# Performance work log

Measured on AMD Instinct MI355X. Metric: run time of the kernel, lower is better.

## Reference

```python
import jax, jax.numpy as jnp
import numpy as np

M = 8        # number of input features
NMF = 4      # membership functions per feature
R = NMF ** M # 65536 rules
N = 1024     # batch size


def setup_inputs() -> dict:
    key = jax.random.key(0)
    k1, k2, k3, k4, k5 = jax.random.split(key, 5)
    x = jax.random.normal(k1, (N, M), dtype=jnp.float32)
    # Antecedent parameters: torch.rand -> uniform [0,1)
    center = jax.random.uniform(k2, (M, NMF), dtype=jnp.float32)
    sigma = jax.random.uniform(k3, (M, NMF), dtype=jnp.float32)
    # Consequent linear layer, init_Consequent uses uniform [0,1)
    W = jax.random.uniform(k4, (R, M), dtype=jnp.float32)
    b = jax.random.uniform(k5, (R,), dtype=jnp.float32)
    return {"x": x, "center": center, "sigma": sigma, "W": W, "b": b}


def reference(x, center, sigma, W, b):
    # droprule=False (deterministic reference; the torch drop_rule is random Bernoulli masking)
    n = x.shape[0]
    # Gaussian membership, faithful to torch: exp(-(x - c)^2 / 2 * sigma^2)
    # mg: [N, M, NMF]
    mg = jnp.exp(-((x[:, :, None] - center[None, :, :]) ** 2) * 0.5 * (sigma[None, :, :] ** 2))
    # Combinatorial rule product via mixed-radix broadcasting:
    # fg[n, r] = prod_m mg[n, m, digit_m(r)], feature 0 most significant.
    fg = mg[:, 0, :]  # [N, NMF]
    for m in range(1, M):
        fg = (fg[:, :, None] * mg[:, m, None, :]).reshape(n, -1)
    # fg: [N, R]
    fg_bar = fg / jnp.sum(fg, axis=1, keepdims=True)
    rule_out = x @ W.T + b  # [N, R]
    return jnp.sum(fg_bar * rule_out, axis=1)  # [N]
```

## Files before the change

kernel.cpp:

```cpp
#include <hip/hip_runtime.h>
#include <hip/hip_bf16.h>

typedef __attribute__((ext_vector_type(8))) short short8;
typedef __attribute__((ext_vector_type(4))) float f32x4;

#define KB 16

__device__ __forceinline__ ushort f2bf(float f) {
    __hip_bfloat16 h = __float2bfloat16(f);
    return *reinterpret_cast<ushort*>(&h);
}
__device__ __forceinline__ unsigned pk2(float a, float b) {
    return (unsigned)f2bf(a) | ((unsigned)f2bf(b) << 16);
}

__global__ __launch_bounds__(256) void fz_main(
    const float* __restrict__ x, const float* __restrict__ center,
    const float* __restrict__ sigma, const float* __restrict__ W,
    const float* __restrict__ b, float* __restrict__ out, int N)
{
    __shared__ float  xs[16][9];
    __shared__ float  mgs[16][33];
    __shared__ float  pr[16][20] __attribute__((aligned(16)));
    __shared__ ushort plf[8][64][8] __attribute__((aligned(16)));
    __shared__ float  phs[KB][20] __attribute__((aligned(16)));
    __shared__ float  red[4][16][9];
    __shared__ ushort wstg[2][32][16][8] __attribute__((aligned(16)));

    const int t = threadIdx.x;
    const int tile = blockIdx.x >> 4;
    const int kb = blockIdx.x & (KB - 1);

    if (t < 128) {
        int s = t >> 3, m = t & 7;
        xs[s][m] = x[(size_t)(tile * 16 + s) * 8 + m];
    }
    __syncthreads();
    #pragma unroll
    for (int v = 0; v < 2; ++v) {
        int id = t + v * 256;
        int s = id >> 5, i = id & 31, m = i >> 2;
        float d = xs[s][m] - center[i];
        float sg = sigma[i];
        mgs[s][i] = __expf(-d * d * 0.5f * sg * sg);
    }
    __syncthreads();
    {
        int s = t >> 4, a = t & 15;
        pr[s][a] = mgs[s][24 + (a >> 2)] * mgs[s][28 + (a & 3)];
    }
    {
        int hil = t >> 4, s = t & 15;
        int hi = kb * KB + hil;
        phs[hil][s] = mgs[s][hi >> 6] * mgs[s][4 + ((hi >> 4) & 3)]
                    * mgs[s][8 + ((hi >> 2) & 3)] * mgs[s][12 + (hi & 3)];
    }
    __syncthreads();
    {
        const int ls = t >> 5;
        #pragma unroll
        for (int oct = 0; oct < 2; ++oct) {
            const int lane_e = (2 * t + oct) & 63;
            const int s = lane_e & 15;
            const int hi3 = lane_e >> 4;
            const int L0 = ls * 32 + hi3 * 8;
            const float pqv = mgs[s][16 + (L0 >> 6)] * mgs[s][20 + ((L0 >> 4) & 3)];
            const int b7 = L0 & 8;
            const float4 r0 = *reinterpret_cast<const float4*>(&pr[s][b7]);
            const float4 r1 = *reinterpret_cast<const float4*>(&pr[s][b7 + 4]);
            unsigned Pk[4] = { pk2(pqv * r0.x, pqv * r0.y), pk2(pqv * r0.z, pqv * r0.w),
                               pk2(pqv * r1.x, pqv * r1.y), pk2(pqv * r1.z, pqv * r1.w) };
            *reinterpret_cast<short8*>(&plf[ls][lane_e][0]) =
                *reinterpret_cast<short8*>(&Pk[0]);
        }
    }

    const int wv = t >> 6, lane = t & 63;
    const int c = lane & 15, kb4 = lane >> 4;
    const int srow = t >> 1, shalf = (t & 1) * 4;

    auto stage_load = [&](int hil, float4& va, float4& vb, float& bv) {
        const float* wp = W + (size_t)(kb * KB + hil) * 2048;
        va = *reinterpret_cast<const float4*>(wp + t * 4);
        vb = *reinterpret_cast<const float4*>(wp + 1024 + t * 4);
        bv = b[(kb * KB + hil) * 256 + t];
    };
    auto stage_write = [&](int bf, const float4& va, const float4& vb, float bv) {
        ushort* p0 = &wstg[bf][srow >> 3][shalf][srow & 7];
        p0[0] = f2bf(va.x); p0[8] = f2bf(va.y); p0[16] = f2bf(va.z); p0[24] = f2bf(va.w);
        ushort* p1 = &wstg[bf][16 + (srow >> 3)][shalf][srow & 7];
        p1[0] = f2bf(vb.x); p1[8] = f2bf(vb.y); p1[16] = f2bf(vb.z); p1[24] = f2bf(vb.w);
        wstg[bf][t >> 3][8][t & 7] = f2bf(bv);
    };

    __syncthreads();
    short8 A0 = *reinterpret_cast<const short8*>(&plf[2 * wv][lane][0]);
    short8 A1 = *reinterpret_cast<const short8*>(&plf[2 * wv + 1][lane][0]);

    float4 va, vb2; float bv;
    stage_load(0, va, vb2, bv);
    stage_write(0, va, vb2, bv);
    __syncthreads();

    f32x4 master = {0.f, 0.f, 0.f, 0.f};
    #pragma unroll 2
    for (int hil = 0; hil < KB; ++hil) {
        const int bf = hil & 1;
        if (hil + 1 < KB) stage_load(hil + 1, va, vb2, bv);
        f32x4 d = {0.f, 0.f, 0.f, 0.f};
        short8 B0 = *reinterpret_cast<const short8*>(&wstg[bf][(2 * wv) * 4 + kb4][c][0]);
        short8 B1 = *reinterpret_cast<const short8*>(&wstg[bf][(2 * wv + 1) * 4 + kb4][c][0]);
        d = __builtin_amdgcn_mfma_f32_16x16x32_bf16(A0, B0, d, 0, 0, 0);
        d = __builtin_amdgcn_mfma_f32_16x16x32_bf16(A1, B1, d, 0, 0, 0);
        const float4 phv = *reinterpret_cast<const float4*>(&phs[hil][kb4 * 4]);
        master[0] += phv.x * d[0]; master[1] += phv.y * d[1];
        master[2] += phv.z * d[2]; master[3] += phv.w * d[3];
        if (hil + 1 < KB) stage_write(bf ^ 1, va, vb2, bv);
        __syncthreads();
    }

    if (c < 9) {
        #pragma unroll
        for (int r = 0; r < 4; ++r)
            red[wv][kb4 * 4 + r][c] = master[r];
    }
    __syncthreads();
    if (t < 144) {
        int s = t / 9, cc = t % 9;
        red[0][s][cc] += red[1][s][cc] + red[2][s][cc] + red[3][s][cc];
    }
    __syncthreads();
    if (t < 16) {
        const int s = t;
        float denom = 1.f;
        #pragma unroll
        for (int m = 0; m < 8; ++m)
            denom *= (mgs[s][4 * m] + mgs[s][4 * m + 1] +
                      mgs[s][4 * m + 2] + mgs[s][4 * m + 3]);
        float num = red[0][s][8];
        #pragma unroll
        for (int m = 0; m < 8; ++m) num += xs[s][m] * red[0][s][m];
        atomicAdd(&out[tile * 16 + s], num / denom);
    }
}

extern "C" void kernel_launch(void* const* d_in, const int* in_sizes, int n_in,
                              void* d_out, int out_size, void* d_ws, size_t ws_size,
                              hipStream_t stream)
{
    const float* x      = (const float*)d_in[0];
    const float* center = (const float*)d_in[1];
    const float* sigma  = (const float*)d_in[2];
    const float* W      = (const float*)d_in[3];
    const float* b      = (const float*)d_in[4];
    float* out = (float*)d_out;
    const int N = in_sizes[0] / 8;

    hipMemsetAsync(out, 0, (size_t)out_size * sizeof(float), stream);
    fz_main<<<(N / 16) * KB, 256, 0, stream>>>(x, center, sigma, W, b, out, N);
}
```

Before: 74.27 us.

## Give each wavefront private weight staging to drop per-iteration block barriers

Each wavefront now stages only the weight rows its own MFMAs consume, in a padded per-wave LDS region, so the per-iteration __syncthreads in the main loop is removed. The A operands are built directly in registers rather than through an LDS round trip, and the x staging buffer and its barrier are replaced by direct global reads. This cuts block-wide synchronisation and LDS traffic. It relies on intra-wavefront lockstep for LDS write/read ordering within the double buffer, which is a correctness risk without explicit wave-level fences.

```diff
diff --git a/kernel.cpp b/kernel.cpp
--- a/kernel.cpp
+++ b/kernel.cpp
@@ -19,28 +19,22 @@
     const float* __restrict__ sigma, const float* __restrict__ W,
     const float* __restrict__ b, float* __restrict__ out, int N)
 {
-    __shared__ float  xs[16][9];
     __shared__ float  mgs[16][33];
-    __shared__ float  pr[16][20] __attribute__((aligned(16)));
-    __shared__ ushort plf[8][64][8] __attribute__((aligned(16)));
+    __shared__ float  pr[16][20]  __attribute__((aligned(16)));
     __shared__ float  phs[KB][20] __attribute__((aligned(16)));
     __shared__ float  red[4][16][9];
-    __shared__ ushort wstg[2][32][16][8] __attribute__((aligned(16)));
+    __shared__ ushort wstg[4][2][8][17][8] __attribute__((aligned(16)));
 
     const int t = threadIdx.x;
     const int tile = blockIdx.x >> 4;
     const int kb = blockIdx.x & (KB - 1);
 
-    if (t < 128) {
-        int s = t >> 3, m = t & 7;
-        xs[s][m] = x[(size_t)(tile * 16 + s) * 8 + m];
-    }
-    __syncthreads();
     #pragma unroll
     for (int v = 0; v < 2; ++v) {
         int id = t + v * 256;
         int s = id >> 5, i = id & 31, m = i >> 2;
-        float d = xs[s][m] - center[i];
+        float xv = x[(size_t)(tile * 16 + s) * 8 + m];
+        float d = xv - center[i];
         float sg = sigma[i];
         mgs[s][i] = __expf(-d * d * 0.5f * sg * sg);
     }
@@ -56,67 +50,62 @@
                     * mgs[s][8 + ((hi >> 2) & 3)] * mgs[s][12 + (hi & 3)];
     }
     __syncthreads();
+
+    const int wv = t >> 6, lane = t & 63;
+    const int c = lane & 15, kb4 = lane >> 4;
+
+    short8 A[2];
     {
-        const int ls = t >> 5;
+        const int s_a = lane & 15;
         #pragma unroll
-        for (int oct = 0; oct < 2; ++oct) {
-            const int lane_e = (2 * t + oct) & 63;
-            const int s = lane_e & 15;
-            const int hi3 = lane_e >> 4;
-            const int L0 = ls * 32 + hi3 * 8;
-            const float pqv = mgs[s][16 + (L0 >> 6)] * mgs[s][20 + ((L0 >> 4) & 3)];
+        for (int q = 0; q < 2; ++q) {
+            const int ls = 2 * wv + q;
+            const int L0 = ls * 32 + kb4 * 8;
+            const float pq = mgs[s_a][16 + (L0 >> 6)] * mgs[s_a][20 + ((L0 >> 4) & 3)];
             const int b7 = L0 & 8;
-            const float4 r0 = *reinterpret_cast<const float4*>(&pr[s][b7]);
-            const float4 r1 = *reinterpret_cast<const float4*>(&pr[s][b7 + 4]);
-            unsigned Pk[4] = { pk2(pqv * r0.x, pqv * r0.y), pk2(pqv * r0.z, pqv * r0.w),
-                               pk2(pqv * r1.x, pqv * r1.y), pk2(pqv * r1.z, pqv * r1.w) };
-            *reinterpret_cast<short8*>(&plf[ls][lane_e][0]) =
-                *reinterpret_cast<short8*>(&Pk[0]);
+            const float4 r0 = *reinterpret_cast<const float4*>(&pr[s_a][b7]);
+            const float4 r1 = *reinterpret_cast<const float4*>(&pr[s_a][b7 + 4]);
+            unsigned Pk[4] = { pk2(pq * r0.x, pq * r0.y), pk2(pq * r0.z, pq * r0.w),
+                               pk2(pq * r1.x, pq * r1.y), pk2(pq * r1.z, pq * r1.w) };
+            A[q] = *reinterpret_cast<short8*>(&Pk[0]);
         }
     }
 
-    const int wv = t >> 6, lane = t & 63;
-    const int c = lane & 15, kb4 = lane >> 4;
-    const int srow = t >> 1, shalf = (t & 1) * 4;
+    const float*  wrow = W + ((size_t)kb * 4096 + 64 * wv + lane) * 8;
+    const float*  brow = b + kb * 4096 + 64 * wv + lane;
+    ushort* rg = &wstg[wv][0][0][0][0];
 
-    auto stage_load = [&](int hil, float4& va, float4& vb, float& bv) {
-        const float* wp = W + (size_t)(kb * KB + hil) * 2048;
-        va = *reinterpret_cast<const float4*>(wp + t * 4);
-        vb = *reinterpret_cast<const float4*>(wp + 1024 + t * 4);
-        bv = b[(kb * KB + hil) * 256 + t];
+    auto sload = [&](int hil, float4& wa, float4& wb, float& bv) {
+        wa = *reinterpret_cast<const float4*>(wrow + hil * 2048);
+        wb = *reinterpret_cast<const float4*>(wrow + hil * 2048 + 4);
+        bv = brow[hil * 256];
     };
-    auto stage_write = [&](int bf, const float4& va, const float4& vb, float bv) {
-        ushort* p0 = &wstg[bf][srow >> 3][shalf][srow & 7];
-        p0[0] = f2bf(va.x); p0[8] = f2bf(va.y); p0[16] = f2bf(va.z); p0[24] = f2bf(va.w);
-        ushort* p1 = &wstg[bf][16 + (srow >> 3)][shalf][srow & 7];
-        p1[0] = f2bf(vb.x); p1[8] = f2bf(vb.y); p1[16] = f2bf(vb.z); p1[24] = f2bf(vb.w);
-        wstg[bf][t >> 3][8][t & 7] = f2bf(bv);
+    auto swrite = [&](int buf, const float4& wa, const float4& wb, float bv) {
+        ushort* p = rg + buf * 1088 + (lane >> 3) * 136 + (lane & 7);
+        p[0]  = f2bf(wa.x); p[8]  = f2bf(wa.y); p[16] = f2bf(wa.z); p[24] = f2bf(wa.w);
+        p[32] = f2bf(wb.x); p[40] = f2bf(wb.y); p[48] = f2bf(wb.z); p[56] = f2bf(wb.w);
+        p[64] = f2bf(bv);
     };
 
-    __syncthreads();
-    short8 A0 = *reinterpret_cast<const short8*>(&plf[2 * wv][lane][0]);
-    short8 A1 = *reinterpret_cast<const short8*>(&plf[2 * wv + 1][lane][0]);
-
-    float4 va, vb2; float bv;
-    stage_load(0, va, vb2, bv);
-    stage_write(0, va, vb2, bv);
-    __syncthreads();
+    float4 wa, wb2; float bv;
+    sload(0, wa, wb2, bv);
+    swrite(0, wa, wb2, bv);
 
     f32x4 master = {0.f, 0.f, 0.f, 0.f};
-    #pragma unroll 2
+    #pragma unroll 4
     for (int hil = 0; hil < KB; ++hil) {
-        const int bf = hil & 1;
-        if (hil + 1 < KB) stage_load(hil + 1, va, vb2, bv);
+        const int buf = hil & 1;
+        if (hil + 1 < KB) sload(hil + 1, wa, wb2, bv);
+        const ushort* q = rg + buf * 1088 + kb4 * 136 + c * 8;
+        short8 B0 = *reinterpret_cast<const short8*>(q);
+        short8 B1 = *reinterpret_cast<const short8*>(q + 4 * 136);
         f32x4 d = {0.f, 0.f, 0.f, 0.f};
-        short8 B0 = *reinterpret_cast<const short8*>(&wstg[bf][(2 * wv) * 4 + kb4][c][0]);
-        short8 B1 = *reinterpret_cast<const short8*>(&wstg[bf][(2 * wv + 1) * 4 + kb4][c][0]);
-        d = __builtin_amdgcn_mfma_f32_16x16x32_bf16(A0, B0, d, 0, 0, 0);
-        d = __builtin_amdgcn_mfma_f32_16x16x32_bf16(A1, B1, d, 0, 0, 0);
+        d = __builtin_amdgcn_mfma_f32_16x16x32_bf16(A[0], B0, d, 0, 0, 0);
+        d = __builtin_amdgcn_mfma_f32_16x16x32_bf16(A[1], B1, d, 0, 0, 0);
         const float4 phv = *reinterpret_cast<const float4*>(&phs[hil][kb4 * 4]);
         master[0] += phv.x * d[0]; master[1] += phv.y * d[1];
         master[2] += phv.z * d[2]; master[3] += phv.w * d[3];
-        if (hil + 1 < KB) stage_write(bf ^ 1, va, vb2, bv);
-        __syncthreads();
+        if (hil + 1 < KB) swrite(buf ^ 1, wa, wb2, bv);
     }
 
     if (c < 9) {
@@ -139,7 +128,8 @@
                       mgs[s][4 * m + 2] + mgs[s][4 * m + 3]);
         float num = red[0][s][8];
         #pragma unroll
-        for (int m = 0; m < 8; ++m) num += xs[s][m] * red[0][s][m];
+        for (int m = 0; m < 8; ++m)
+            num += x[(size_t)(tile * 16 + s) * 8 + m] * red[0][s][m];
         atomicAdd(&out[tile * 16 + s], num / denom);
     }
 }
```

Result: faster. 71.00 us (-4.4%).
